# Kernel tuning notes

Measured on AMD Instinct MI355X. Metric: run time of the kernel, lower is better.

Reference implementation:

```python
import jax, jax.numpy as jnp
import numpy as np

NUM_LEARNERS = 50000
NUM_SCENES = 2000
EMBED_DIM = 128
SPARSITY = 0.1


def setup_inputs() -> dict:
    key = jax.random.key(0)
    k_m, k_w1, k_b1, k_w2, k_b2 = jax.random.split(key, 5)
    m = jax.random.uniform(k_m, (NUM_LEARNERS, NUM_SCENES), dtype=jnp.float32)
    m = jnp.where(m < SPARSITY, m, 0.0)
    return {
        "normalized_matrix": m,
        "W1": jax.random.normal(k_w1, (1, 16), dtype=jnp.float32),
        "b1": jax.random.normal(k_b1, (16,), dtype=jnp.float32),
        "W2": jax.random.normal(k_w2, (16, EMBED_DIM), dtype=jnp.float32),
        "b2": jax.random.normal(k_b2, (EMBED_DIM,), dtype=jnp.float32),
    }


def reference(normalized_matrix, W1, b1, W2, b2):
    # The torch module feeds the nonzero COLUMN INDICES (as floats) of each row
    # into MLP(1->16->d) and mean-pools. Since the MLP input is just the index j,
    # precompute mlp_out[j] for all scenes once, then a masked matmul + count
    # division gives the per-row mean over nonzero positions.
    num_scenes = normalized_matrix.shape[1]
    idx = jnp.arange(num_scenes, dtype=normalized_matrix.dtype)[:, None]  # [S, 1]
    h = jax.nn.relu(idx @ W1 + b1)                                        # [S, 16]
    mlp_out = h @ W2 + b2                                                 # [S, d]

    mask = (normalized_matrix != 0).astype(normalized_matrix.dtype)       # [L, S]
    counts = mask.sum(axis=1, keepdims=True)                              # [L, 1]
    # rows with zero nonzeros yield an all-zero mask row -> zero embedding,
    # matching the torch zeros fallback; clamp denominator to avoid 0/0.
    emb = (mask @ mlp_out) / jnp.maximum(counts, 1.0)                     # [L, d]
    return emb
```

## Files before the change

### kernel.cpp

```cpp
#include <hip/hip_runtime.h>

#define NUM_LEARNERS 50000
#define NUM_SCENES   2000
#define EMBED_DIM    128
#define HID          16

__global__ __launch_bounds__(256) void fused_gather_mean_kernel(
    const float* __restrict__ M,
    const float* __restrict__ W1, const float* __restrict__ b1,
    const float* __restrict__ W2, const float* __restrict__ b2,
    float* __restrict__ out)
{
    __shared__ unsigned short idxbuf[4][NUM_SCENES];
    const int  wave = threadIdx.x >> 6;
    const int  lane = threadIdx.x & 63;
    const long row  = (long)blockIdx.x * 4 + wave;

    const int g   = lane >> 2;
    const int sub = lane & 3;
    float w1v[4], b1v[4];
#pragma unroll
    for (int c = 0; c < 4; ++c) {
        w1v[c] = W1[4 * sub + c];
        b1v[c] = b1[4 * sub + c];
    }

    const float4* __restrict__ M4 = (const float4*)(M + row * NUM_SCENES);
    unsigned short* myidx = idxbuf[wave];

    int count = 0;
#pragma unroll
    for (int it = 0; it < 8; ++it) {
        int c4 = it * 64 + lane;
        float4 v = make_float4(0.f, 0.f, 0.f, 0.f);
        if (c4 < 500) v = M4[c4];
        float vals[4] = {v.x, v.y, v.z, v.w};
#pragma unroll
        for (int c = 0; c < 4; ++c) {
            bool nz = (vals[c] != 0.0f);
            unsigned long long m = __ballot(nz);
            if (nz) {
                int below = __builtin_amdgcn_mbcnt_hi(
                    (unsigned)(m >> 32),
                    __builtin_amdgcn_mbcnt_lo((unsigned)m, 0));
                myidx[count + below] = (unsigned short)(c4 * 4 + c);
            }
            count += __popcll(m);
        }
    }

    __syncthreads();

    float4 acc = make_float4(0.f, 0.f, 0.f, 0.f);
#pragma unroll 2
    for (int n = 0; n < count; n += 16) {
        int   i     = n + g;
        bool  valid = (i < count);
        int   isafe = valid ? i : 0;
        float x     = (float)myidx[isafe];
        float mval  = valid ? 1.0f : 0.0f;
#pragma unroll
        for (int c = 0; c < 4; ++c) {
            float h = fmaxf(fmaf(x, w1v[c], b1v[c]), 0.0f);
            (&acc.x)[c] = fmaf(h, mval, (&acc.x)[c]);
        }
    }

#pragma unroll
    for (int off = 4; off < 64; off <<= 1) {
        acc.x += __shfl_xor(acc.x, off);
        acc.y += __shfl_xor(acc.y, off);
        acc.z += __shfl_xor(acc.z, off);
        acc.w += __shfl_xor(acc.w, off);
    }
    float s[HID];
#pragma unroll
    for (int a = 0; a < 4; ++a) {
        s[4 * a + 0] = __shfl(acc.x, a);
        s[4 * a + 1] = __shfl(acc.y, a);
        s[4 * a + 2] = __shfl(acc.z, a);
        s[4 * a + 3] = __shfl(acc.w, a);
    }

    const float cnt = (float)count;
    const float inv = 1.0f / fmaxf(cnt, 1.0f);
    const float2* __restrict__ W2v = (const float2*)W2;
    float2 bv = ((const float2*)b2)[lane];
    float e0 = cnt * bv.x;
    float e1 = cnt * bv.y;
#pragma unroll
    for (int k = 0; k < HID; ++k) {
        float2 w = W2v[k * 64 + lane];
        e0 = fmaf(s[k], w.x, e0);
        e1 = fmaf(s[k], w.y, e1);
    }
    ((float2*)out)[row * 64 + lane] = make_float2(e0 * inv, e1 * inv);
}

extern "C" void kernel_launch(void* const* d_in, const int* in_sizes, int n_in,
                              void* d_out, int out_size, void* d_ws, size_t ws_size,
                              hipStream_t stream) {
    const float* M  = (const float*)d_in[0];
    const float* W1 = (const float*)d_in[1];
    const float* b1 = (const float*)d_in[2];
    const float* W2 = (const float*)d_in[3];
    const float* b2 = (const float*)d_in[4];
    float* out = (float*)d_out;

    fused_gather_mean_kernel<<<NUM_LEARNERS / 4, 256, 0, stream>>>(
        M, W1, b1, W2, b2, out);
}
```

Baseline: 534.5 us.

## Replace index gather with bitmap prefix sums and closed-form ReLU threshold sums

Each wave now builds a 2000-bit nonzero bitmap per row with ballots and computes prefix counts and prefix index sums by shuffle scans. Because the first MLP layer is linear in the index j, each hidden unit's ReLU sum is w*sum(j)+b*count over the indices on the active side of a threshold, which is read from the prefix sums. This removes the shared-memory index buffer, the __syncthreads, and the per-nonzero accumulation loop. In exchange it adds scalar loads instead of float4 loads and more ALU work on popcounts. The threshold arithmetic also risks float rounding differences at the boundary.

New measurement: 522.8 us. 2.2% less time.

```diff
diff --git a/kernel.cpp b/kernel.cpp
--- a/kernel.cpp
+++ b/kernel.cpp
@@ -5,84 +5,87 @@
 #define EMBED_DIM    128
 #define HID          16
 
-__global__ __launch_bounds__(256) void fused_gather_mean_kernel(
+__device__ __forceinline__ int wpc32(unsigned x) {
+    return __popc(x & 0xAAAAAAAAu)        + (__popc(x & 0xCCCCCCCCu) << 1)
+         + (__popc(x & 0xF0F0F0F0u) << 2) + (__popc(x & 0xFF00FF00u) << 3)
+         + (__popc(x & 0xFFFF0000u) << 4);
+}
+
+__global__ __launch_bounds__(256) void bitmap_mean_kernel(
     const float* __restrict__ M,
     const float* __restrict__ W1, const float* __restrict__ b1,
     const float* __restrict__ W2, const float* __restrict__ b2,
     float* __restrict__ out)
 {
-    __shared__ unsigned short idxbuf[4][NUM_SCENES];
     const int  wave = threadIdx.x >> 6;
     const int  lane = threadIdx.x & 63;
     const long row  = (long)blockIdx.x * 4 + wave;
+    const float* __restrict__ Mrow = M + row * NUM_SCENES;
 
-    const int g   = lane >> 2;
-    const int sub = lane & 3;
-    float w1v[4], b1v[4];
+    float v[32];
 #pragma unroll
-    for (int c = 0; c < 4; ++c) {
-        w1v[c] = W1[4 * sub + c];
-        b1v[c] = b1[4 * sub + c];
+    for (int G = 0; G < 32; ++G) {
+        int j = (G << 6) + lane;
+        v[G] = (j < NUM_SCENES) ? Mrow[j] : 0.0f;
     }
 
-    const float4* __restrict__ M4 = (const float4*)(M + row * NUM_SCENES);
-    unsigned short* myidx = idxbuf[wave];
-
-    int count = 0;
+    int vml = 0, vmh = 0;
 #pragma unroll
-    for (int it = 0; it < 8; ++it) {
-        int c4 = it * 64 + lane;
-        float4 v = make_float4(0.f, 0.f, 0.f, 0.f);
-        if (c4 < 500) v = M4[c4];
-        float vals[4] = {v.x, v.y, v.z, v.w};
-#pragma unroll
-        for (int c = 0; c < 4; ++c) {
-            bool nz = (vals[c] != 0.0f);
-            unsigned long long m = __ballot(nz);
-            if (nz) {
-                int below = __builtin_amdgcn_mbcnt_hi(
-                    (unsigned)(m >> 32),
-                    __builtin_amdgcn_mbcnt_lo((unsigned)m, 0));
-                myidx[count + below] = (unsigned short)(c4 * 4 + c);
-            }
-            count += __popcll(m);
+    for (int G = 0; G < 32; ++G) {
+        unsigned long long bm = __ballot(v[G] != 0.0f);
+        if (lane == G) {
+            vml = (int)(unsigned)bm;
+            vmh = (int)(unsigned)(bm >> 32);
         }
     }
 
-    __syncthreads();
+    unsigned ml = (unsigned)vml, mh = (unsigned)vmh;
+    int pc = __popc(ml) + __popc(mh);
+    int Sg = wpc32(ml) + wpc32(mh) + (__popc(mh) << 5) + ((lane & 31) << 6) * pc;
+    if (lane >= 32) { pc = 0; Sg = 0; }
 
-    float4 acc = make_float4(0.f, 0.f, 0.f, 0.f);
-#pragma unroll 2
-    for (int n = 0; n < count; n += 16) {
-        int   i     = n + g;
-        bool  valid = (i < count);
-        int   isafe = valid ? i : 0;
-        float x     = (float)myidx[isafe];
-        float mval  = valid ? 1.0f : 0.0f;
+    int sp = pc, ss = Sg;
 #pragma unroll
-        for (int c = 0; c < 4; ++c) {
-            float h = fmaxf(fmaf(x, w1v[c], b1v[c]), 0.0f);
-            (&acc.x)[c] = fmaf(h, mval, (&acc.x)[c]);
-        }
+    for (int s = 1; s < 64; s <<= 1) {
+        int idx = lane + s; idx = idx > 63 ? 63 : idx;
+        sp += __shfl(sp, idx);
+        ss += __shfl(ss, idx);
     }
+    const int Ctot = __shfl(sp, 0);
+    const int Stot = __shfl(ss, 0);
 
+    int kk = lane & 15;
+    float w = W1[kk], b = b1[kk];
+    float t = -b / (w != 0.0f ? w : 1.0f);
+    t = fminf(fmaxf(t, -1.0f), 2001.0f);
+    int c;
+    if (w > 0.0f)      c = (int)floorf(t) + 1;
+    else if (w < 0.0f) c = (int)ceilf(t);
+    else               c = (b > 0.0f) ? 0 : NUM_SCENES;
+    c = c < 0 ? 0 : (c > NUM_SCENES ? NUM_SCENES : c);
+
+    int gb = c >> 6, l0 = c & 63;
+    unsigned bl = (unsigned)__shfl(vml, gb);
+    unsigned bh = (unsigned)__shfl(vmh, gb);
+    int nidx = gb + 1;
+    int CSn = __shfl(sp, nidx);
+    int SSn = __shfl(ss, nidx);
+    unsigned long long pm = (((unsigned long long)bh << 32) | bl) >> l0;
+    unsigned pml = (unsigned)pm, pmh = (unsigned)(pm >> 32);
+    int pcp  = __popc(pml) + __popc(pmh);
+    int wpcp = wpc32(pml) + wpc32(pmh) + (__popc(pmh) << 5);
+    int Cge = CSn + pcp;
+    int Sge = SSn + c * pcp + wpcp;
+
+    float sigma = (w >= 0.0f)
+        ? (w * (float)Sge + b * (float)Cge)
+        : (w * (float)(Stot - Sge) + b * (float)(Ctot - Cge));
+
+    float s16[HID];
 #pragma unroll
-    for (int off = 4; off < 64; off <<= 1) {
-        acc.x += __shfl_xor(acc.x, off);
-        acc.y += __shfl_xor(acc.y, off);
-        acc.z += __shfl_xor(acc.z, off);
-        acc.w += __shfl_xor(acc.w, off);
-    }
-    float s[HID];
-#pragma unroll
-    for (int a = 0; a < 4; ++a) {
-        s[4 * a + 0] = __shfl(acc.x, a);
-        s[4 * a + 1] = __shfl(acc.y, a);
-        s[4 * a + 2] = __shfl(acc.z, a);
-        s[4 * a + 3] = __shfl(acc.w, a);
-    }
+    for (int k = 0; k < HID; ++k) s16[k] = __shfl(sigma, k);
 
-    const float cnt = (float)count;
+    const float cnt = (float)Ctot;
     const float inv = 1.0f / fmaxf(cnt, 1.0f);
     const float2* __restrict__ W2v = (const float2*)W2;
     float2 bv = ((const float2*)b2)[lane];
@@ -90,9 +93,9 @@
     float e1 = cnt * bv.y;
 #pragma unroll
     for (int k = 0; k < HID; ++k) {
-        float2 w = W2v[k * 64 + lane];
-        e0 = fmaf(s[k], w.x, e0);
-        e1 = fmaf(s[k], w.y, e1);
+        float2 wv = W2v[k * 64 + lane];
+        e0 = fmaf(s16[k], wv.x, e0);
+        e1 = fmaf(s16[k], wv.y, e1);
     }
     ((float2*)out)[row * 64 + lane] = make_float2(e0 * inv, e1 * inv);
 }
@@ -107,6 +110,6 @@
     const float* b2 = (const float*)d_in[4];
     float* out = (float*)d_out;
 
-    fused_gather_mean_kernel<<<NUM_LEARNERS / 4, 256, 0, stream>>>(
+    bitmap_mean_kernel<<<NUM_LEARNERS / 4, 256, 0, stream>>>(
         M, W1, b1, W2, b2, out);
 }
```
